# Kernel tuning notes

Hardware: AMD Instinct MI355X
Metric: run time of the kernel (lower is better)

Reference implementation:

```python
import jax, jax.numpy as jnp
import numpy as np

ATTR_W = 1.0   # attraction_weight
REP_W = 1.0    # repulsion_weight
K_INST = 64    # max number of slice (instance) ids per event


def setup_inputs() -> dict:
    key = jax.random.key(0)
    k1, k2, k3, k4 = jax.random.split(key, 4)
    B, N, D = 4, 4096, 8
    beta = jax.random.normal(k1, (B, N, 1), dtype=jnp.float32)
    embed = jax.random.normal(k2, (B, N, D), dtype=jnp.float32)
    slice_id = jax.random.randint(k3, (B, N), 0, K_INST)
    is_cp = jax.random.randint(k4, (B, N), 0, 2)
    return {"beta": beta, "embed": embed, "slice_id": slice_id, "is_cp": is_cp}


def _per_batch(beta_b, emb_b, sid, cp):
    # beta_b: [N], emb_b: [N, D], sid: [N] int, cp: [N] int
    N = beta_b.shape[0]
    cp_mask = cp == 1
    y = cp_mask.astype(beta_b.dtype)
    pos = jnp.sum(y)
    neg = N - pos
    valid = (pos >= 1) & (neg >= 1)
    # beta BCE-with-logits with detached pos_weight = neg/pos
    pos_weight = jax.lax.stop_gradient(neg / (pos + 1e-6))
    bce = jnp.mean(pos_weight * y * jax.nn.softplus(-beta_b)
                   + (1.0 - y) * jax.nn.softplus(beta_b))
    # attraction: per instance, mean squared distance to first CP hit of that instance
    idx = jnp.arange(N)
    first_cp = jax.ops.segment_min(jnp.where(cp_mask, idx, N), sid, num_segments=K_INST)
    has_cp = first_cp < N                                   # [K]
    cp_emb = emb_b[jnp.clip(first_cp, 0, N - 1)]            # [K, D]
    d2 = jnp.sum((emb_b - cp_emb[sid]) ** 2, axis=-1)       # [N]
    seg_sum = jax.ops.segment_sum(d2, sid, num_segments=K_INST)
    counts = jax.ops.segment_sum(jnp.ones((N,), beta_b.dtype), sid, num_segments=K_INST)
    inst_mean = jnp.where((counts > 0) & has_cp, seg_sum / jnp.maximum(counts, 1.0), 0.0)
    attr = jnp.sum(inst_mean) * ATTR_W
    # repulsion: mean of exp(-d2) over all CP x CP pairs (diagonal included)
    sq = jnp.sum(emb_b * emb_b, axis=-1)                    # [N]
    d2p = jnp.maximum(sq[:, None] + sq[None, :] - 2.0 * (emb_b @ emb_b.T), 0.0)  # [N, N]
    rep_sum = jnp.sum(jnp.exp(-d2p) * (y[:, None] * y[None, :]))
    rep = jnp.where(pos > 1, rep_sum / jnp.maximum(pos * pos, 1.0), 0.0) * REP_W
    total = bce + attr + rep
    return jnp.where(valid, total, 0.0), valid.astype(beta_b.dtype)


def reference(beta, embed, slice_id, is_cp):
    beta2 = beta.squeeze(-1)                                # [B, N]
    totals, valids = jax.vmap(_per_batch)(beta2, embed, slice_id, is_cp)
    count = jnp.sum(valids)
    return jnp.where(count > 0, jnp.sum(totals) / jnp.maximum(count, 1.0), 0.0)
```

## Files before the change

kernel.cpp:

```cpp
#include <hip/hip_runtime.h>
#include <math.h>

#define BB 4
#define NN 4096
#define KK 64
#define GA 8
#define IT 1024
#define JT 32
#define NTI (NN / IT)
#define NTJ (NN / JT)
#define KC_BLOCKS (BB * NTI * NTJ)

__global__ __launch_bounds__(512) void kA(
    const float* __restrict__ beta, const float* __restrict__ embed,
    const int* __restrict__ sid_g, const int* __restrict__ cp_g,
    float* __restrict__ cpemb, float* __restrict__ cpsq,
    float* __restrict__ gA1, float* __restrict__ gA2,
    float* __restrict__ gpos, int* __restrict__ gfirst,
    int* __restrict__ gcounts, int* __restrict__ cpcount)
{
    const int b   = blockIdx.x >> 3;
    const int sub = blockIdx.x & 7;
    const int t    = threadIdx.x;
    const int lane = t & 63;
    const int wid  = t >> 6;

    __shared__ int   s_first[KK], s_counts[KK], s_wc[8], s_off[8], s_base;
    __shared__ float r1[8], r2[8], r3[8];

    if (t < KK) { s_first[t] = NN; s_counts[t] = 0; }
    __syncthreads();

    const int i = sub * 512 + t;
    const float* emb_b = embed + (size_t)b * NN * 8;

    int   sid = sid_g[(size_t)b * NN + i];
    int   cp  = cp_g[(size_t)b * NN + i];
    float bt  = beta[(size_t)b * NN + i];
    bool  is1 = (cp == 1);

    float l  = __logf(1.f + __expf(-fabsf(bt)));
    float a1 = is1 ? (l + fmaxf(-bt, 0.f)) : 0.f;
    float a2 = is1 ? 0.f : (l + fmaxf(bt, 0.f));
    float pf = is1 ? 1.f : 0.f;

    if (is1) atomicMin(&s_first[sid], i);
    atomicAdd(&s_counts[sid], 1);

    unsigned long long m = __ballot(is1);
    if (lane == 0) s_wc[wid] = __popcll(m);

    #pragma unroll
    for (int o = 32; o > 0; o >>= 1) {
        a1 += __shfl_down(a1, o);
        a2 += __shfl_down(a2, o);
        pf += __shfl_down(pf, o);
    }
    if (lane == 0) { r1[wid] = a1; r2[wid] = a2; r3[wid] = pf; }
    __syncthreads();

    if (t == 0) {
        float A1 = 0.f, A2 = 0.f, P = 0.f;
        int run = 0;
        #pragma unroll
        for (int w = 0; w < 8; ++w) {
            A1 += r1[w]; A2 += r2[w]; P += r3[w];
            s_off[w] = run; run += s_wc[w];
        }
        s_base = atomicAdd(&cpcount[b], run);
        atomicAdd(&gA1[b], A1);
        atomicAdd(&gA2[b], A2);
        atomicAdd(&gpos[b], P);
    }
    __syncthreads();

    if (is1) {
        int slot = s_base + s_off[wid] + __popcll(m & ((1ull << lane) - 1ull));
        const float4* ep = (const float4*)(emb_b + (size_t)i * 8);
        float4 e0 = ep[0], e1 = ep[1];
        float sq = e0.x*e0.x + e0.y*e0.y + e0.z*e0.z + e0.w*e0.w
                 + e1.x*e1.x + e1.y*e1.y + e1.z*e1.z + e1.w*e1.w;
        const float S = 1.41421356237f;
        float4* op = (float4*)(cpemb + ((size_t)b * NN + slot) * 8);
        op[0] = make_float4(e0.x*S, e0.y*S, e0.z*S, e0.w*S);
        op[1] = make_float4(e1.x*S, e1.y*S, e1.z*S, e1.w*S);
        cpsq[(size_t)b * NN + slot] = sq;
    }

    if (t < KK) {
        atomicMin(&gfirst[b * KK + t], s_first[t]);
        int c = s_counts[t];
        if (c) atomicAdd(&gcounts[b * KK + t], c);
    }
}

__global__ __launch_bounds__(256) void kB(
    const float* __restrict__ embed, const int* __restrict__ sid_g,
    const int* __restrict__ gfirst, float* __restrict__ seg)
{
    const int b   = blockIdx.x >> 4;
    const int blk = blockIdx.x & 15;
    const int t   = threadIdx.x;

    __shared__ float s_fe[KK][8];
    __shared__ float s_seg[KK];

    const float* emb_b = embed + (size_t)b * NN * 8;
    if (t < KK) {
        s_seg[t] = 0.f;
        int f = gfirst[b * KK + t];
        if (f > NN - 1) f = NN - 1;
        const float4* fp = (const float4*)(emb_b + (size_t)f * 8);
        *(float4*)&s_fe[t][0] = fp[0];
        *(float4*)&s_fe[t][4] = fp[1];
    }
    __syncthreads();

    int i = blk * 256 + t;
    int sid = sid_g[(size_t)b * NN + i];
    const float4* ep = (const float4*)(emb_b + (size_t)i * 8);
    float4 e0 = ep[0], e1 = ep[1];
    float4 f0 = *(const float4*)&s_fe[sid][0];
    float4 f1 = *(const float4*)&s_fe[sid][4];
    float dx, d2 = 0.f;
    dx = e0.x - f0.x; d2 += dx * dx;
    dx = e0.y - f0.y; d2 += dx * dx;
    dx = e0.z - f0.z; d2 += dx * dx;
    dx = e0.w - f0.w; d2 += dx * dx;
    dx = e1.x - f1.x; d2 += dx * dx;
    dx = e1.y - f1.y; d2 += dx * dx;
    dx = e1.z - f1.z; d2 += dx * dx;
    dx = e1.w - f1.w; d2 += dx * dx;
    atomicAdd(&s_seg[sid], d2);
    __syncthreads();
    if (t < KK) atomicAdd(&seg[b * KK + t], s_seg[t]);
}

__global__ __launch_bounds__(256) void kC(
    const float* __restrict__ cpemb, const float* __restrict__ cpsq,
    const int* __restrict__ cpcount, float* __restrict__ rep)
{
    const int blk = blockIdx.x;
    const int b   = blk >> 9;
    const int rem = blk & 511;
    const int it  = rem >> 7;
    const int jt  = rem & 127;
    const int t   = threadIdx.x;

    const int pos = cpcount[b];
    if (it * IT >= pos || jt * JT >= pos) return;

    __shared__ float s_je[JT * 8];
    __shared__ float s_jq[JT];
    __shared__ float r[4];

    int jn = pos - jt * JT; if (jn > JT) jn = JT;
    const float* cpe_b = cpemb + (size_t)b * NN * 8;
    const float* cpq_b = cpsq + (size_t)b * NN;

    if (t < 64) {
        int row = t >> 1, half = t & 1;
        if (row < jn) {
            *(float4*)&s_je[row * 8 + half * 4] =
                *(const float4*)(cpe_b + (size_t)(jt * JT + row) * 8 + half * 4);
            if (half == 0) s_jq[row] = cpq_b[jt * JT + row];
        }
    }
    __syncthreads();

    float4 e0[4], e1[4];
    float  nq[4];
    #pragma unroll
    for (int u = 0; u < 4; ++u) {
        int i = it * IT + u * 256 + t;
        bool iv = (i < pos);
        const float4* ip = (const float4*)(cpe_b + (size_t)(iv ? i : 0) * 8);
        e0[u] = ip[0]; e1[u] = ip[1];
        nq[u] = iv ? -cpq_b[i] : -1e30f;
    }

    float sum = 0.f;
    #pragma unroll 2
    for (int j = 0; j < jn; ++j) {
        float4 f0 = *(const float4*)&s_je[j * 8];
        float4 f1 = *(const float4*)&s_je[j * 8 + 4];
        float qj = s_jq[j];
        #pragma unroll
        for (int u = 0; u < 4; ++u) {
            float arg = nq[u] - qj;
            arg = fmaf(e0[u].x, f0.x, arg);
            arg = fmaf(e0[u].y, f0.y, arg);
            arg = fmaf(e0[u].z, f0.z, arg);
            arg = fmaf(e0[u].w, f0.w, arg);
            arg = fmaf(e1[u].x, f1.x, arg);
            arg = fmaf(e1[u].y, f1.y, arg);
            arg = fmaf(e1[u].z, f1.z, arg);
            arg = fmaf(e1[u].w, f1.w, arg);
            arg = fminf(arg, 0.f);
            sum += __expf(arg);
        }
    }
    #pragma unroll
    for (int o = 32; o > 0; o >>= 1) sum += __shfl_down(sum, o);
    if ((t & 63) == 0) r[t >> 6] = sum;
    __syncthreads();
    if (t == 0) atomicAdd(&rep[b], r[0] + r[1] + r[2] + r[3]);
}

__global__ __launch_bounds__(64) void kD(
    const int* __restrict__ gfirst, const int* __restrict__ gcounts,
    const float* __restrict__ seg, const float* __restrict__ gA1,
    const float* __restrict__ gA2, const float* __restrict__ gpos,
    const float* __restrict__ rep, float* __restrict__ out)
{
    const int k = threadIdx.x;
    float tot = 0.f, cnt = 0.f;
    for (int b = 0; b < BB; ++b) {
        int f   = gfirst[b * KK + k];
        int c   = gcounts[b * KK + k];
        float s = seg[b * KK + k];
        float attr = (c > 0 && f < NN) ? s / (float)c : 0.f;
        #pragma unroll
        for (int o = 32; o > 0; o >>= 1) attr += __shfl_down(attr, o);
        if (k == 0) {
            float P = gpos[b];
            float neg = (float)NN - P;
            bool valid = (P >= 1.f) && (neg >= 1.f);
            float bce = (neg / (P + 1e-6f) * gA1[b] + gA2[b]) * (1.f / (float)NN);
            float rp = (P > 1.f) ? rep[b] / fmaxf(P * P, 1.f) : 0.f;
            float ttl = bce + attr + rp;
            if (valid) { tot += ttl; cnt += 1.f; }
        }
    }
    if (k == 0) out[0] = (cnt > 0.f) ? tot / cnt : 0.f;
}

extern "C" void kernel_launch(void* const* d_in, const int* in_sizes, int n_in,
                              void* d_out, int out_size, void* d_ws, size_t ws_size,
                              hipStream_t stream) {
    const float* beta     = (const float*)d_in[0];
    const float* embed    = (const float*)d_in[1];
    const int*   slice_id = (const int*)d_in[2];
    const int*   is_cp    = (const int*)d_in[3];
    float* out = (float*)d_out;

    float* cpemb = (float*)d_ws;
    float* cpsq  = cpemb + (size_t)BB * NN * 8;
    float* gA1   = cpsq + (size_t)BB * NN;
    float* gA2   = gA1 + BB;
    float* gpos  = gA2 + BB;
    float* rep   = gpos + BB;
    float* seg   = rep + BB;
    int* gcounts = (int*)(seg + BB * KK);
    int* cpcount = gcounts + BB * KK;
    int* gfirst  = cpcount + BB;

    size_t zero_bytes = (size_t)(4 * BB + 2 * BB * KK + BB) * 4;
    hipMemsetAsync(gA1, 0, zero_bytes, stream);
    hipMemsetAsync(gfirst, 0x7F, BB * KK * 4, stream);

    kA<<<BB * GA, 512, 0, stream>>>(beta, embed, slice_id, is_cp,
                                    cpemb, cpsq, gA1, gA2, gpos,
                                    gfirst, gcounts, cpcount);
    kB<<<BB * 16, 256, 0, stream>>>(embed, slice_id, gfirst, seg);
    kC<<<KC_BLOCKS, 256, 0, stream>>>(cpemb, cpsq, cpcount, rep);
    kD<<<1, 64, 0, stream>>>(gfirst, gcounts, seg, gA1, gA2, gpos, rep, out);
}
```

Before: 89.69 us.

## Fuse all loss stages into one cooperative kernel with grid-wide syncs

Replaces the four separate kernels and two memsets with a single cooperative kernel that uses grid.sync between phases. Phase one gives each batch to a single block, which computes BCE, per-instance first-CP, attraction sums and CP compaction in shared memory, so global atomics and cross-kernel handoff go away. Phase two spreads the CP×CP repulsion over 256 blocks that loop over tiles, and one block writes the final reduction. The aim is to remove launch and memset overhead. In exchange, phase one runs on only four blocks and the repulsion phase has much less parallelism and occupancy than the earlier 2048-block grid.

```diff
diff --git a/kernel.cpp b/kernel.cpp
--- a/kernel.cpp
+++ b/kernel.cpp
@@ -1,238 +1,240 @@
 #include <hip/hip_runtime.h>
+#include <hip/hip_cooperative_groups.h>
 #include <math.h>
+
+namespace cg = cooperative_groups;
 
 #define BB 4
 #define NN 4096
 #define KK 64
-#define GA 8
-#define IT 1024
+#define TPB 256
+#define GRID 256
+#define BPB 64
 #define JT 32
-#define NTI (NN / IT)
-#define NTJ (NN / JT)
-#define KC_BLOCKS (BB * NTI * NTJ)
-
-__global__ __launch_bounds__(512) void kA(
+
+__global__ __launch_bounds__(TPB) void kAll(
     const float* __restrict__ beta, const float* __restrict__ embed,
     const int* __restrict__ sid_g, const int* __restrict__ cp_g,
     float* __restrict__ cpemb, float* __restrict__ cpsq,
-    float* __restrict__ gA1, float* __restrict__ gA2,
-    float* __restrict__ gpos, int* __restrict__ gfirst,
-    int* __restrict__ gcounts, int* __restrict__ cpcount)
+    float* __restrict__ gbase, float* __restrict__ gpos,
+    float* __restrict__ grep, int* __restrict__ gcpn,
+    float* __restrict__ out)
 {
-    const int b   = blockIdx.x >> 3;
-    const int sub = blockIdx.x & 7;
+    cg::grid_group grid = cg::this_grid();
+    const int blk  = blockIdx.x;
     const int t    = threadIdx.x;
     const int lane = t & 63;
     const int wid  = t >> 6;
 
-    __shared__ int   s_first[KK], s_counts[KK], s_wc[8], s_off[8], s_base;
-    __shared__ float r1[8], r2[8], r3[8];
-
-    if (t < KK) { s_first[t] = NN; s_counts[t] = 0; }
-    __syncthreads();
-
-    const int i = sub * 512 + t;
-    const float* emb_b = embed + (size_t)b * NN * 8;
-
-    int   sid = sid_g[(size_t)b * NN + i];
-    int   cp  = cp_g[(size_t)b * NN + i];
-    float bt  = beta[(size_t)b * NN + i];
-    bool  is1 = (cp == 1);
-
-    float l  = __logf(1.f + __expf(-fabsf(bt)));
-    float a1 = is1 ? (l + fmaxf(-bt, 0.f)) : 0.f;
-    float a2 = is1 ? 0.f : (l + fmaxf(bt, 0.f));
-    float pf = is1 ? 1.f : 0.f;
-
-    if (is1) atomicMin(&s_first[sid], i);
-    atomicAdd(&s_counts[sid], 1);
-
-    unsigned long long m = __ballot(is1);
-    if (lane == 0) s_wc[wid] = __popcll(m);
-
-    #pragma unroll
-    for (int o = 32; o > 0; o >>= 1) {
-        a1 += __shfl_down(a1, o);
-        a2 += __shfl_down(a2, o);
-        pf += __shfl_down(pf, o);
-    }
-    if (lane == 0) { r1[wid] = a1; r2[wid] = a2; r3[wid] = pf; }
-    __syncthreads();
-
-    if (t == 0) {
-        float A1 = 0.f, A2 = 0.f, P = 0.f;
-        int run = 0;
-        #pragma unroll
-        for (int w = 0; w < 8; ++w) {
-            A1 += r1[w]; A2 += r2[w]; P += r3[w];
-            s_off[w] = run; run += s_wc[w];
-        }
-        s_base = atomicAdd(&cpcount[b], run);
-        atomicAdd(&gA1[b], A1);
-        atomicAdd(&gA2[b], A2);
-        atomicAdd(&gpos[b], P);
-    }
-    __syncthreads();
-
-    if (is1) {
-        int slot = s_base + s_off[wid] + __popcll(m & ((1ull << lane) - 1ull));
-        const float4* ep = (const float4*)(emb_b + (size_t)i * 8);
-        float4 e0 = ep[0], e1 = ep[1];
-        float sq = e0.x*e0.x + e0.y*e0.y + e0.z*e0.z + e0.w*e0.w
-                 + e1.x*e1.x + e1.y*e1.y + e1.z*e1.z + e1.w*e1.w;
-        const float S = 1.41421356237f;
-        float4* op = (float4*)(cpemb + ((size_t)b * NN + slot) * 8);
-        op[0] = make_float4(e0.x*S, e0.y*S, e0.z*S, e0.w*S);
-        op[1] = make_float4(e1.x*S, e1.y*S, e1.z*S, e1.w*S);
-        cpsq[(size_t)b * NN + slot] = sq;
-    }
-
-    if (t < KK) {
-        atomicMin(&gfirst[b * KK + t], s_first[t]);
-        int c = s_counts[t];
-        if (c) atomicAdd(&gcounts[b * KK + t], c);
-    }
-}
-
-__global__ __launch_bounds__(256) void kB(
-    const float* __restrict__ embed, const int* __restrict__ sid_g,
-    const int* __restrict__ gfirst, float* __restrict__ seg)
-{
-    const int b   = blockIdx.x >> 4;
-    const int blk = blockIdx.x & 15;
-    const int t   = threadIdx.x;
-
+    __shared__ int   s_first[KK];
+    __shared__ int   s_counts[KK];
+    __shared__ float s_seg[KK];
     __shared__ float s_fe[KK][8];
-    __shared__ float s_seg[KK];
-
-    const float* emb_b = embed + (size_t)b * NN * 8;
-    if (t < KK) {
-        s_seg[t] = 0.f;
-        int f = gfirst[b * KK + t];
-        if (f > NN - 1) f = NN - 1;
-        const float4* fp = (const float4*)(emb_b + (size_t)f * 8);
-        *(float4*)&s_fe[t][0] = fp[0];
-        *(float4*)&s_fe[t][4] = fp[1];
-    }
-    __syncthreads();
-
-    int i = blk * 256 + t;
-    int sid = sid_g[(size_t)b * NN + i];
-    const float4* ep = (const float4*)(emb_b + (size_t)i * 8);
-    float4 e0 = ep[0], e1 = ep[1];
-    float4 f0 = *(const float4*)&s_fe[sid][0];
-    float4 f1 = *(const float4*)&s_fe[sid][4];
-    float dx, d2 = 0.f;
-    dx = e0.x - f0.x; d2 += dx * dx;
-    dx = e0.y - f0.y; d2 += dx * dx;
-    dx = e0.z - f0.z; d2 += dx * dx;
-    dx = e0.w - f0.w; d2 += dx * dx;
-    dx = e1.x - f1.x; d2 += dx * dx;
-    dx = e1.y - f1.y; d2 += dx * dx;
-    dx = e1.z - f1.z; d2 += dx * dx;
-    dx = e1.w - f1.w; d2 += dx * dx;
-    atomicAdd(&s_seg[sid], d2);
-    __syncthreads();
-    if (t < KK) atomicAdd(&seg[b * KK + t], s_seg[t]);
-}
-
-__global__ __launch_bounds__(256) void kC(
-    const float* __restrict__ cpemb, const float* __restrict__ cpsq,
-    const int* __restrict__ cpcount, float* __restrict__ rep)
-{
-    const int blk = blockIdx.x;
-    const int b   = blk >> 9;
-    const int rem = blk & 511;
-    const int it  = rem >> 7;
-    const int jt  = rem & 127;
-    const int t   = threadIdx.x;
-
-    const int pos = cpcount[b];
-    if (it * IT >= pos || jt * JT >= pos) return;
-
+    __shared__ float s_red[3][4];
+    __shared__ int   s_cpn;
     __shared__ float s_je[JT * 8];
     __shared__ float s_jq[JT];
-    __shared__ float r[4];
-
-    int jn = pos - jt * JT; if (jn > JT) jn = JT;
-    const float* cpe_b = cpemb + (size_t)b * NN * 8;
-    const float* cpq_b = cpsq + (size_t)b * NN;
-
-    if (t < 64) {
-        int row = t >> 1, half = t & 1;
-        if (row < jn) {
-            *(float4*)&s_je[row * 8 + half * 4] =
-                *(const float4*)(cpe_b + (size_t)(jt * JT + row) * 8 + half * 4);
-            if (half == 0) s_jq[row] = cpq_b[jt * JT + row];
+    __shared__ float s_r[4];
+
+    if (blk < BB) {
+        const int b = blk;
+        if (t < KK) { s_first[t] = NN; s_counts[t] = 0; s_seg[t] = 0.f; }
+        if (t == 0) s_cpn = 0;
+        __syncthreads();
+
+        const int4*   sid4p = (const int4*)(sid_g + (size_t)b * NN);
+        const int4*   cp4p  = (const int4*)(cp_g + (size_t)b * NN);
+        const float4* b4p   = (const float4*)(beta + (size_t)b * NN);
+        const float*  emb_b = embed + (size_t)b * NN * 8;
+
+        int4 sids[4];
+        int  slots[16];
+        float a1 = 0.f, a2 = 0.f;
+        int posl = 0;
+
+        #pragma unroll
+        for (int k = 0; k < 4; ++k) {
+            int idx4 = k * TPB + t;
+            int4 s4 = sid4p[idx4];
+            int4 c4 = cp4p[idx4];
+            float4 bt4 = b4p[idx4];
+            sids[k] = s4;
+            int base_i = idx4 * 4;
+            float bts[4] = {bt4.x, bt4.y, bt4.z, bt4.w};
+            int   cps[4] = {c4.x, c4.y, c4.z, c4.w};
+            int   ssd[4] = {s4.x, s4.y, s4.z, s4.w};
+            #pragma unroll
+            for (int e = 0; e < 4; ++e) {
+                bool is1 = (cps[e] == 1);
+                float bt = bts[e];
+                float l = __logf(1.f + __expf(-fabsf(bt)));
+                if (is1) {
+                    a1 += l + fmaxf(-bt, 0.f);
+                    posl++;
+                    atomicMin(&s_first[ssd[e]], base_i + e);
+                } else {
+                    a2 += l + fmaxf(bt, 0.f);
+                }
+                atomicAdd(&s_counts[ssd[e]], 1);
+                unsigned long long m = __ballot(is1);
+                int wbase = 0;
+                if (lane == 0 && m != 0ull) wbase = atomicAdd(&s_cpn, __popcll(m));
+                wbase = __shfl(wbase, 0);
+                slots[k * 4 + e] = is1 ? (wbase + __popcll(m & ((1ull << lane) - 1ull))) : -1;
+            }
+        }
+
+        float pf = (float)posl;
+        #pragma unroll
+        for (int o = 32; o > 0; o >>= 1) {
+            a1 += __shfl_down(a1, o);
+            a2 += __shfl_down(a2, o);
+            pf += __shfl_down(pf, o);
+        }
+        if (lane == 0) { s_red[0][wid] = a1; s_red[1][wid] = a2; s_red[2][wid] = pf; }
+        __syncthreads();
+
+        if (t < KK) {
+            int f = s_first[t]; if (f > NN - 1) f = NN - 1;
+            const float4* fp = (const float4*)(emb_b + (size_t)f * 8);
+            *(float4*)&s_fe[t][0] = fp[0];
+            *(float4*)&s_fe[t][4] = fp[1];
+        }
+        __syncthreads();
+
+        float* cpe_b = cpemb + (size_t)b * NN * 8;
+        float* cpq_b = cpsq + (size_t)b * NN;
+        const float S = 1.41421356237f;
+        #pragma unroll
+        for (int k = 0; k < 4; ++k) {
+            int ssd[4] = {sids[k].x, sids[k].y, sids[k].z, sids[k].w};
+            #pragma unroll
+            for (int e = 0; e < 4; ++e) {
+                int i = (k * TPB + t) * 4 + e;
+                const float4* ep = (const float4*)(emb_b + (size_t)i * 8);
+                float4 e0 = ep[0], e1 = ep[1];
+                float4 f0 = *(float4*)&s_fe[ssd[e]][0];
+                float4 f1 = *(float4*)&s_fe[ssd[e]][4];
+                float dx, d2 = 0.f;
+                dx = e0.x - f0.x; d2 += dx * dx;
+                dx = e0.y - f0.y; d2 += dx * dx;
+                dx = e0.z - f0.z; d2 += dx * dx;
+                dx = e0.w - f0.w; d2 += dx * dx;
+                dx = e1.x - f1.x; d2 += dx * dx;
+                dx = e1.y - f1.y; d2 += dx * dx;
+                dx = e1.z - f1.z; d2 += dx * dx;
+                dx = e1.w - f1.w; d2 += dx * dx;
+                atomicAdd(&s_seg[ssd[e]], d2);
+                int sl = slots[k * 4 + e];
+                if (sl >= 0) {
+                    float sq = e0.x*e0.x + e0.y*e0.y + e0.z*e0.z + e0.w*e0.w
+                             + e1.x*e1.x + e1.y*e1.y + e1.z*e1.z + e1.w*e1.w;
+                    float4* op = (float4*)(cpe_b + (size_t)sl * 8);
+                    op[0] = make_float4(e0.x*S, e0.y*S, e0.z*S, e0.w*S);
+                    op[1] = make_float4(e1.x*S, e1.y*S, e1.z*S, e1.w*S);
+                    cpq_b[sl] = sq;
+                }
+            }
+        }
+        __syncthreads();
+
+        if (t < KK) {
+            int c = s_counts[t], f = s_first[t];
+            float attr = (c > 0 && f < NN) ? s_seg[t] / (float)c : 0.f;
+            #pragma unroll
+            for (int o = 32; o > 0; o >>= 1) attr += __shfl_down(attr, o);
+            if (t == 0) {
+                float A1 = s_red[0][0] + s_red[0][1] + s_red[0][2] + s_red[0][3];
+                float A2 = s_red[1][0] + s_red[1][1] + s_red[1][2] + s_red[1][3];
+                float P  = s_red[2][0] + s_red[2][1] + s_red[2][2] + s_red[2][3];
+                float neg = (float)NN - P;
+                float bce = (neg / (P + 1e-6f) * A1 + A2) * (1.f / (float)NN);
+                gbase[b] = bce + attr;
+                gpos[b]  = P;
+                grep[b]  = 0.f;
+                gcpn[b]  = s_cpn;
+            }
         }
     }
-    __syncthreads();
-
-    float4 e0[4], e1[4];
-    float  nq[4];
-    #pragma unroll
-    for (int u = 0; u < 4; ++u) {
-        int i = it * IT + u * 256 + t;
-        bool iv = (i < pos);
-        const float4* ip = (const float4*)(cpe_b + (size_t)(iv ? i : 0) * 8);
-        e0[u] = ip[0]; e1[u] = ip[1];
-        nq[u] = iv ? -cpq_b[i] : -1e30f;
+
+    grid.sync();
+
+    {
+        const int b2  = blk >> 6;
+        const int jt0 = blk & 63;
+        const int pos = gcpn[b2];
+        const float* cpe2 = cpemb + (size_t)b2 * NN * 8;
+        const float* cpq2 = cpsq + (size_t)b2 * NN;
+
+        float sum = 0.f;
+        for (int jbase = jt0 * JT; jbase < pos; jbase += BPB * JT) {
+            int jn = pos - jbase; if (jn > JT) jn = JT;
+            __syncthreads();
+            if (t < 64) {
+                int row = t >> 1, half = t & 1;
+                if (row < jn) {
+                    *(float4*)&s_je[row * 8 + half * 4] =
+                        *(const float4*)(cpe2 + (size_t)(jbase + row) * 8 + half * 4);
+                    if (half == 0) s_jq[row] = cpq2[jbase + row];
+                }
+            }
+            __syncthreads();
+
+            for (int ibase = 0; ibase < pos; ibase += TPB * 4) {
+                float4 e0[4], e1[4];
+                float  nq[4];
+                #pragma unroll
+                for (int u = 0; u < 4; ++u) {
+                    int i = ibase + u * TPB + t;
+                    bool iv = (i < pos);
+                    const float4* ip = (const float4*)(cpe2 + (size_t)(iv ? i : 0) * 8);
+                    e0[u] = ip[0]; e1[u] = ip[1];
+                    nq[u] = iv ? -cpq2[i] : -1e30f;
+                }
+                #pragma unroll 2
+                for (int j = 0; j < jn; ++j) {
+                    float4 f0 = *(const float4*)&s_je[j * 8];
+                    float4 f1 = *(const float4*)&s_je[j * 8 + 4];
+                    float qj = s_jq[j];
+                    #pragma unroll
+                    for (int u = 0; u < 4; ++u) {
+                        float arg = nq[u] - qj;
+                        arg = fmaf(e0[u].x, f0.x, arg);
+                        arg = fmaf(e0[u].y, f0.y, arg);
+                        arg = fmaf(e0[u].z, f0.z, arg);
+                        arg = fmaf(e0[u].w, f0.w, arg);
+                        arg = fmaf(e1[u].x, f1.x, arg);
+                        arg = fmaf(e1[u].y, f1.y, arg);
+                        arg = fmaf(e1[u].z, f1.z, arg);
+                        arg = fmaf(e1[u].w, f1.w, arg);
+                        arg = fminf(arg, 0.f);
+                        sum += __expf(arg);
+                    }
+                }
+            }
+        }
+        #pragma unroll
+        for (int o = 32; o > 0; o >>= 1) sum += __shfl_down(sum, o);
+        if (lane == 0) s_r[wid] = sum;
+        __syncthreads();
+        if (t == 0) atomicAdd(&grep[b2], s_r[0] + s_r[1] + s_r[2] + s_r[3]);
     }
 
-    float sum = 0.f;
-    #pragma unroll 2
-    for (int j = 0; j < jn; ++j) {
-        float4 f0 = *(const float4*)&s_je[j * 8];
-        float4 f1 = *(const float4*)&s_je[j * 8 + 4];
-        float qj = s_jq[j];
-        #pragma unroll
-        for (int u = 0; u < 4; ++u) {
-            float arg = nq[u] - qj;
-            arg = fmaf(e0[u].x, f0.x, arg);
-            arg = fmaf(e0[u].y, f0.y, arg);
-            arg = fmaf(e0[u].z, f0.z, arg);
-            arg = fmaf(e0[u].w, f0.w, arg);
-            arg = fmaf(e1[u].x, f1.x, arg);
-            arg = fmaf(e1[u].y, f1.y, arg);
-            arg = fmaf(e1[u].z, f1.z, arg);
-            arg = fmaf(e1[u].w, f1.w, arg);
-            arg = fminf(arg, 0.f);
-            sum += __expf(arg);
-        }
-    }
-    #pragma unroll
-    for (int o = 32; o > 0; o >>= 1) sum += __shfl_down(sum, o);
-    if ((t & 63) == 0) r[t >> 6] = sum;
-    __syncthreads();
-    if (t == 0) atomicAdd(&rep[b], r[0] + r[1] + r[2] + r[3]);
-}
-
-__global__ __launch_bounds__(64) void kD(
-    const int* __restrict__ gfirst, const int* __restrict__ gcounts,
-    const float* __restrict__ seg, const float* __restrict__ gA1,
-    const float* __restrict__ gA2, const float* __restrict__ gpos,
-    const float* __restrict__ rep, float* __restrict__ out)
-{
-    const int k = threadIdx.x;
-    float tot = 0.f, cnt = 0.f;
-    for (int b = 0; b < BB; ++b) {
-        int f   = gfirst[b * KK + k];
-        int c   = gcounts[b * KK + k];
-        float s = seg[b * KK + k];
-        float attr = (c > 0 && f < NN) ? s / (float)c : 0.f;
-        #pragma unroll
-        for (int o = 32; o > 0; o >>= 1) attr += __shfl_down(attr, o);
-        if (k == 0) {
+    grid.sync();
+
+    if (blk == 0 && t == 0) {
+        float tot = 0.f, cnt = 0.f;
+        #pragma unroll
+        for (int b = 0; b < BB; ++b) {
             float P = gpos[b];
             float neg = (float)NN - P;
             bool valid = (P >= 1.f) && (neg >= 1.f);
-            float bce = (neg / (P + 1e-6f) * gA1[b] + gA2[b]) * (1.f / (float)NN);
-            float rp = (P > 1.f) ? rep[b] / fmaxf(P * P, 1.f) : 0.f;
-            float ttl = bce + attr + rp;
+            float rp = (P > 1.f) ? grep[b] / fmaxf(P * P, 1.f) : 0.f;
+            float ttl = gbase[b] + rp;
             if (valid) { tot += ttl; cnt += 1.f; }
         }
+        out[0] = (cnt > 0.f) ? tot / cnt : 0.f;
     }
-    if (k == 0) out[0] = (cnt > 0.f) ? tot / cnt : 0.f;
 }
 
 extern "C" void kernel_launch(void* const* d_in, const int* in_sizes, int n_in,
@@ -246,23 +248,13 @@
 
     float* cpemb = (float*)d_ws;
     float* cpsq  = cpemb + (size_t)BB * NN * 8;
-    float* gA1   = cpsq + (size_t)BB * NN;
-    float* gA2   = gA1 + BB;
-    float* gpos  = gA2 + BB;
-    float* rep   = gpos + BB;
-    float* seg   = rep + BB;
-    int* gcounts = (int*)(seg + BB * KK);
-    int* cpcount = gcounts + BB * KK;
-    int* gfirst  = cpcount + BB;
-
-    size_t zero_bytes = (size_t)(4 * BB + 2 * BB * KK + BB) * 4;
-    hipMemsetAsync(gA1, 0, zero_bytes, stream);
-    hipMemsetAsync(gfirst, 0x7F, BB * KK * 4, stream);
-
-    kA<<<BB * GA, 512, 0, stream>>>(beta, embed, slice_id, is_cp,
-                                    cpemb, cpsq, gA1, gA2, gpos,
-                                    gfirst, gcounts, cpcount);
-    kB<<<BB * 16, 256, 0, stream>>>(embed, slice_id, gfirst, seg);
-    kC<<<KC_BLOCKS, 256, 0, stream>>>(cpemb, cpsq, cpcount, rep);
-    kD<<<1, 64, 0, stream>>>(gfirst, gcounts, seg, gA1, gA2, gpos, rep, out);
+    float* gbase = cpsq + (size_t)BB * NN;
+    float* gpos  = gbase + BB;
+    float* grep  = gpos + BB;
+    int*   gcpn  = (int*)(grep + BB);
+
+    void* args[] = { (void*)&beta, (void*)&embed, (void*)&slice_id, (void*)&is_cp,
+                     (void*)&cpemb, (void*)&cpsq, (void*)&gbase, (void*)&gpos,
+                     (void*)&grep, (void*)&gcpn, (void*)&out };
+    hipLaunchCooperativeKernel((void*)kAll, dim3(GRID), dim3(TPB), args, 0, stream);
 }
```

Measured after the change: 152.4 us. 69.9% more time.
